# Kernel tuning notes

Measured on AMD Instinct MI355X. Metric: run time of the kernel, lower is better.

The kernel has to match this reference:

```python
import jax, jax.numpy as jnp
import numpy as np

B, S, D, H, HD = 8, 1374, 384, 6, 64
NUM_PATCHES = 1369  # (518 // 14) ** 2
NUM_PREFIX = 5      # 1 cls + 4 registers


def setup_inputs() -> dict:
    key = jax.random.key(0)
    ks = jax.random.split(key, 10)
    init = 0.02  # truncated_normal(0.02) approximated by scaled normal
    x = jax.random.normal(ks[0], (B, S, D), jnp.float32)
    wq = jax.random.truncated_normal(ks[1], -2.0, 2.0, (D, H, HD), jnp.float32) * init
    wk = jax.random.truncated_normal(ks[2], -2.0, 2.0, (D, H, HD), jnp.float32) * init
    wv = jax.random.truncated_normal(ks[3], -2.0, 2.0, (D, H, HD), jnp.float32) * init
    wo = jax.random.truncated_normal(ks[4], -2.0, 2.0, (H, HD, D), jnp.float32) * init
    bq = jnp.zeros((H, HD), jnp.float32)
    bk = jnp.zeros((H, HD), jnp.float32)
    bv = jnp.zeros((H, HD), jnp.float32)
    bo = jnp.zeros((D,), jnp.float32)
    keep_patch_indices = jax.random.randint(ks[5], (B, NUM_PATCHES), 0, NUM_PATCHES).astype(jnp.int64)
    return {"x": x, "wq": wq, "bq": bq, "wk": wk, "bk": bk, "wv": wv, "bv": bv,
            "wo": wo, "bo": bo, "keep_patch_indices": keep_patch_indices, "k_patches": 685}


def reference(x, wq, bq, wk, bk, wv, bv, wo, bo, keep_patch_indices, k_patches):
    # q/k/v projections: DenseGeneral to (heads, head_dim)
    q = jnp.einsum('bsd,dhe->bshe', x, wq) + bq
    k = jnp.einsum('bsd,dhe->bshe', x, wk) + bk
    v = jnp.einsum('bsd,dhe->bshe', x, wv) + bv

    z = jnp.einsum('bqhd,bkhd->bhqk', q / (HD ** 0.5), k)  # [B,H,S,S]
    attn_logits = z  # saved BEFORE masking (used by 'mse' criterion)

    # dynamic scatter mask: patch columns >= k_patches get -inf
    num_selected = keep_patch_indices.shape[1]
    patch_idx = jnp.arange(num_selected)
    indices_to_mask = jnp.where(patch_idx >= k_patches, patch_idx, num_selected) + NUM_PREFIX
    # out-of-bounds indices (== num_selected + NUM_PREFIX) are dropped by JAX scatter semantics
    z = z.at[:, :, :, indices_to_mask].set(-jnp.inf)

    attn_map = jax.nn.softmax(z, axis=-1)
    zo = jnp.einsum('bhqk,bkhd->bqhd', attn_map, v)
    output = jnp.einsum('bqhd,hdo->bqo', zo, wo) + bo  # wo contracts (heads, head_dim)

    # attn_aggregate = ['cls_token','reg_token','patch_token'], zoom_map_criterion='mse'
    am = attn_logits.mean(axis=1)  # mean over heads -> [B,S,S]
    aggs = jnp.stack([
        am[:, 0:1, :].mean(axis=1),      # cls token
        am[:, 1:5, :].mean(axis=1),      # register tokens
        am[:, 5:1374, :].mean(axis=1),   # patch tokens
    ], axis=1)                            # [B,3,S]
    attn_agg = aggs.mean(axis=1)          # [B,S]
    return output, attn_agg
```

## Files before the change

kernel.cpp:

```cpp
#include <hip/hip_runtime.h>
#include <stdint.h>

#define BB 8
#define SS 1374
#define DD 384
#define HH 6
#define HDIM 64
#define MROWS (BB*SS)
#define NPFX 5
#define SPAD 1376

typedef __attribute__((ext_vector_type(8))) short bf16x8;
typedef __attribute__((ext_vector_type(4))) float f32x4;
typedef __attribute__((ext_vector_type(4))) unsigned int u32x4;
typedef u32x4 __attribute__((aligned(4))) u32x4_u;

__device__ __forceinline__ unsigned short f2bf(float f){
  union { float f; unsigned int u; } v; v.f = f;
  return (unsigned short)((v.u + 0x7FFFu + ((v.u >> 16) & 1u)) >> 16);
}
__device__ __forceinline__ float bf2f(unsigned short b){
  union { float f; unsigned int u; } v; v.u = ((unsigned int)b) << 16; return v.f;
}
__device__ __forceinline__ unsigned int pk_bf16(float a, float b){
#if __has_builtin(__builtin_amdgcn_cvt_pk_bf16_f32)
  typedef __attribute__((ext_vector_type(2))) __bf16 bfv2;
  bfv2 p = __builtin_amdgcn_cvt_pk_bf16_f32(a, b);
  union { bfv2 v; unsigned int u; } c; c.v = p; return c.u;
#else
  return (unsigned int)f2bf(a) | ((unsigned int)f2bf(b) << 16);
#endif
}

__device__ __forceinline__ int xcd_remap(int i, int n){
  int q = n >> 3, r = n & 7;
  int x = i & 7, j = i >> 3;
  return (x < r ? x*(q+1) : r*(q+1) + (x - r)*q) + j;
}

__global__ void k_prep(const float* __restrict__ x, unsigned short* __restrict__ xb,
                       float* __restrict__ xbar){
  int b = blockIdx.x / 86, ch = blockIdx.x % 86;
  int d = threadIdx.x;
  int s0 = ch*16, s1 = s0 + 16; if (s1 > SS) s1 = SS;
  float acc = 0.f;
  for (int s = s0; s < s1; ++s){
    float v = x[((size_t)b*SS + s)*DD + d];
    float w = (s == 0) ? (1.f/3.f) : (s < 5) ? (1.f/12.f) : (1.f/4107.f);
    acc += w * v;
    xb[((size_t)b*SS + s)*DD + d] = f2bf(v);
  }
  atomicAdd(&xbar[b*DD + d], acc);
}

__global__ __launch_bounds__(256) void k_wtrans(const float* __restrict__ wq,
    const float* __restrict__ wk, const float* __restrict__ wv, const float* __restrict__ wo,
    unsigned short* __restrict__ wbT, unsigned short* __restrict__ woT){
  __shared__ float tile[32][33];
  int bid = blockIdx.x;
  int m = bid / 144, tl = bid % 144;
  int tr = tl / 12, tc = tl % 12;
  const float* src = (m==0) ? wq : (m==1) ? wk : (m==2) ? wv : wo;
  unsigned short* dst = (m < 3) ? (wbT + (size_t)m*384*384) : woT;
  int t = threadIdx.x, c = t & 31, r0 = t >> 5;
  #pragma unroll
  for (int p = 0; p < 4; ++p){
    int r = p*8 + r0;
    tile[r][c] = src[(size_t)(tr*32 + r)*384 + tc*32 + c];
  }
  __syncthreads();
  #pragma unroll
  for (int p = 0; p < 4; ++p){
    int r = p*8 + r0;
    dst[(size_t)(tc*32 + r)*384 + tr*32 + c] = f2bf(tile[c][r]);
  }
}

__global__ void k_qbar(const float* __restrict__ xbar, const float* __restrict__ wq,
                       const float* __restrict__ bq, float* __restrict__ qbar){
  __shared__ float xs[DD];
  int b = blockIdx.x / 6, nc = blockIdx.x % 6;
  int t = threadIdx.x;
  for (int i = t; i < DD; i += 64) xs[i] = xbar[b*DD + i];
  __syncthreads();
  int n = nc*64 + t;
  float acc = bq[n];
  for (int d = 0; d < DD; ++d) acc += xs[d]*wq[(size_t)d*384 + n];
  qbar[b*384 + n] = acc;
}

template<int MODE>
__global__ __launch_bounds__(256) void k_gemm(
    const unsigned short* __restrict__ A, const unsigned short* __restrict__ Bt,
    const float* __restrict__ b0, const float* __restrict__ b1, const float* __restrict__ b2,
    unsigned short* __restrict__ qg, unsigned short* __restrict__ kgp,
    unsigned short* __restrict__ vt, float* __restrict__ out,
    const int* __restrict__ kpat, const float* __restrict__ qbar, float* __restrict__ oagg)
{
  const int NT = (MODE==0) ? 18 : 6;
  int wg = xcd_remap(blockIdx.x, 86*NT);
  int mt = wg / NT, nt = wg % NT;
  const int t = threadIdx.x;
  const int w = t >> 6, lane = t & 63, quad = lane >> 4, l16 = lane & 15;
  const int wm = w >> 1, wn = w & 1;
  const int m0 = mt*128, n0 = nt*64;

  if (MODE == 0 && nt >= 12){
    int s0r_ = m0 % SS;
    int SKv = NPFX + kpat[0]; if (SKv > SS) SKv = SS; if (SKv < 1) SKv = 1;
    int lo = (SKv + 63) & ~63;
    if (s0r_ >= lo && s0r_ + 127 < SS) return;
  }

  constexpr int SMEM_SH = (MODE==0) ? 13824 : 17408;
  __shared__ unsigned short smem[SMEM_SH];
  unsigned short* As = smem;
  unsigned short* Bs = smem + 9216;
  f32x4 acc[4][2];
  #pragma unroll
  for (int i=0;i<4;i++){ acc[i][0] = (f32x4){0,0,0,0}; acc[i][1] = (f32x4){0,0,0,0}; }

  const int ar = t >> 1, akb = (t & 1) * 32;
  int ga = m0 + ar; if (ga > MROWS-1) ga = MROWS-1;
  const unsigned short* ap = A + (size_t)ga*384 + akb;
  const int br = t >> 2, bkb = (t & 3) * 16;
  const unsigned short* bp = Bt + (size_t)(n0 + br)*384 + bkb;

  u32x4 ra[4], rb[2];
  #pragma unroll
  for (int i=0;i<4;i++) ra[i] = *(const u32x4*)(ap + i*8);
  rb[0] = *(const u32x4*)(bp); rb[1] = *(const u32x4*)(bp + 8);

  for (int kc = 0; kc < 6; ++kc){
    asm volatile("s_waitcnt lgkmcnt(0)" ::: "memory");
    __builtin_amdgcn_s_barrier();
    #pragma unroll
    for (int i=0;i<4;i++) *(u32x4*)(As + ar*72 + akb + i*8) = ra[i];
    *(u32x4*)(Bs + br*72 + bkb)     = rb[0];
    *(u32x4*)(Bs + br*72 + bkb + 8) = rb[1];
    asm volatile("s_waitcnt lgkmcnt(0)" ::: "memory");
    __builtin_amdgcn_s_barrier();
    if (kc + 1 < 6){
      int kn = (kc+1)*64;
      #pragma unroll
      for (int i=0;i<4;i++) ra[i] = *(const u32x4*)(ap + kn + i*8);
      rb[0] = *(const u32x4*)(bp + kn); rb[1] = *(const u32x4*)(bp + kn + 8);
    }
    #pragma unroll
    for (int kh = 0; kh < 2; ++kh){
      bf16x8 af[4], bfr[2];
      #pragma unroll
      for (int rf = 0; rf < 4; ++rf)
        af[rf] = *(const bf16x8*)(As + (wm*64 + rf*16 + l16)*72 + kh*32 + quad*8);
      #pragma unroll
      for (int cf = 0; cf < 2; ++cf)
        bfr[cf] = *(const bf16x8*)(Bs + (wn*32 + cf*16 + l16)*72 + kh*32 + quad*8);
      #pragma unroll
      for (int rf = 0; rf < 4; ++rf)
        #pragma unroll
        for (int cf = 0; cf < 2; ++cf)
          acc[rf][cf] = __builtin_amdgcn_mfma_f32_16x16x32_bf16(af[rf], bfr[cf], acc[rf][cf], 0,0,0);
    }
  }

  const int b0r = m0 / SS, s0r = m0 % SS;
  __syncthreads();
  if (MODE == 1){
    float* CsF = (float*)smem;
    #pragma unroll
    for (int cf = 0; cf < 2; ++cf){
      int e = wn*32 + cf*16 + l16;
      float bias = b0[n0 + e];
      #pragma unroll
      for (int rf = 0; rf < 4; ++rf){
        int rr = wm*64 + rf*16 + quad*4;
        #pragma unroll
        for (int r4 = 0; r4 < 4; ++r4)
          CsF[(rr + r4)*68 + e] = acc[rf][cf][r4] + bias;
      }
    }
    __syncthreads();
    #pragma unroll
    for (int p = 0; p < 8; ++p){
      int r = p*16 + (t >> 4), c = t & 15;
      int rr = m0 + r;
      if (rr < MROWS){
        f32x4 v = *(const f32x4*)(CsF + r*68 + c*4);
        *(f32x4*)(out + (size_t)rr*384 + n0 + c*4) = v;
      }
    }
  } else {
    const int mat = nt / 6, h = nt - mat*6;
    const float* bvp = (mat==0) ? b0 : (mat==1) ? b1 : b2;
    const float vsc = (mat==0) ? 0.125f : 1.f;
    if (mat < 2){
      unsigned short* Cs = As;
      unsigned short* dst = (mat==0) ? qg : kgp;
      #pragma unroll
      for (int cf = 0; cf < 2; ++cf){
        int e = wn*32 + cf*16 + l16;
        float bias = bvp[h*64 + e];
        #pragma unroll
        for (int rf = 0; rf < 4; ++rf){
          int rr = wm*64 + rf*16 + quad*4;
          #pragma unroll
          for (int r4 = 0; r4 < 4; ++r4)
            Cs[(rr + r4)*72 + e] = f2bf((acc[rf][cf][r4] + bias)*vsc);
        }
      }
      __syncthreads();
      #pragma unroll
      for (int p = 0; p < 4; ++p){
        int r = p*32 + (t >> 3), c = t & 7;
        int rr = m0 + r;
        if (rr < MROWS){
          int s = s0r + r, bb = b0r;
          if (s >= SS){ s -= SS; ++bb; }
          u32x4 v = *(const u32x4*)(Cs + r*72 + c*8);
          *(u32x4*)(dst + (((size_t)(bb*HH + h))*SS + s)*64 + c*8) = v;
          if (mat == 1){
            const float* qh = qbar + bb*384 + h*64 + c*8;
            float part = 0.f;
            #pragma unroll
            for (int j = 0; j < 4; ++j){
              unsigned int u = v[j];
              part += qh[2*j]     * bf2f((unsigned short)(u & 0xFFFFu));
              part += qh[2*j + 1] * bf2f((unsigned short)(u >> 16));
            }
            part += __shfl_xor(part, 1);
            part += __shfl_xor(part, 2);
            part += __shfl_xor(part, 4);
            if (c == 0) atomicAdd(oagg + bb*SS + s, part * (1.f/48.f));
          }
        }
      }
    } else {
      unsigned short* CsV = As;
      #pragma unroll
      for (int cf = 0; cf < 2; ++cf){
        int e = wn*32 + cf*16 + l16;
        float bias = bvp[h*64 + e];
        #pragma unroll
        for (int rf = 0; rf < 4; ++rf){
          int rr = wm*64 + rf*16 + quad*4;
          #pragma unroll
          for (int p = 0; p < 2; ++p)
            *(unsigned int*)(CsV + e*136 + rr + p*2) =
                pk_bf16(acc[rf][cf][p*2] + bias, acc[rf][cf][p*2+1] + bias);
        }
      }
      __syncthreads();
      const bool nowrap = (s0r + 127 < SS) && (m0 + 127 < MROWS);
      if (nowrap){
        int e = t >> 2;
        unsigned short* vrow = vt + ((size_t)(b0r*HH + h)*64 + e)*SPAD + s0r;
        #pragma unroll
        for (int i = 0; i < 4; ++i){
          int c = (t & 3)*4 + i;
          u32x4 v = *(const u32x4*)(CsV + e*136 + c*8);
          *(u32x4_u*)(vrow + c*8) = v;
        }
      } else {
        for (int idx = t; idx < 64*64; idx += 256){
          int e = idx >> 6, sp = (idx & 63)*2;
          int rr = m0 + sp;
          if (rr < MROWS){
            int s = s0r + sp, bb = b0r;
            if (s >= SS){ s -= SS; ++bb; }
            *(unsigned int*)(vt + ((size_t)(bb*HH + h)*64 + e)*SPAD + s) =
                *(const unsigned int*)(CsV + e*136 + sp);
          }
        }
      }
    }
  }
}

#define KSTR 72
__global__ __launch_bounds__(256) void k_attn(
    const unsigned short* __restrict__ qg, const unsigned short* __restrict__ kg,
    const unsigned short* __restrict__ vt, unsigned short* __restrict__ zo,
    const int* __restrict__ kpat)
{
  const int NQB = 22;
  int wg = xcd_remap(blockIdx.x, 48*NQB);
  int qb = wg % NQB, bh = wg / NQB;
  int t = threadIdx.x, w = t >> 6, lane = t & 63, quad = lane >> 4, l16 = lane & 15;
  int SK = NPFX + kpat[0]; if (SK > SS) SK = SS; if (SK < 1) SK = 1;
  int niter = (SK + 63) >> 6;
  __shared__ unsigned short Ks[2][64*KSTR];
  __shared__ unsigned short Vs[2][64*KSTR];
  __shared__ unsigned short Ps[4][16*KSTR];
  unsigned short* Pw = &Ps[w][0];
  int q0 = qb*64 + w*16;

  bf16x8 aq[2];
  {
    int qrow = q0 + l16; if (qrow > SS-1) qrow = SS-1;
    const unsigned short* p = qg + ((size_t)bh*SS + qrow)*64;
    aq[0] = *(const bf16x8*)(p + quad*8);
    aq[1] = *(const bf16x8*)(p + 32 + quad*8);
  }
  f32x4 o[4];
  float rsum[4] = {0.f,0.f,0.f,0.f};
  #pragma unroll
  for (int i=0;i<4;i++) o[i] = (f32x4){0.f,0.f,0.f,0.f};

  const int srow = t >> 2, sc = (t & 3) * 16;
  const unsigned short* kbase = kg + ((size_t)bh*SS)*64;
  const unsigned short* vbase = vt + ((size_t)bh*64)*SPAD;
  u32x4 rk[2], rv[2];
  {
    rk[0] = *(const u32x4*)(kbase + (size_t)srow*64 + sc);
    rk[1] = *(const u32x4*)(kbase + (size_t)srow*64 + sc + 8);
    rv[0] = *(const u32x4*)(vbase + (size_t)srow*SPAD + sc);
    rv[1] = *(const u32x4*)(vbase + (size_t)srow*SPAD + sc + 8);
  }

  for (int it = 0; it < niter; ++it){
    int k0 = it*64;
    int cur = it & 1;
    unsigned short* Ksc = &Ks[cur][0];
    unsigned short* Vsc = &Vs[cur][0];
    *(u32x4*)(Ksc + srow*KSTR + sc)     = rk[0];
    *(u32x4*)(Ksc + srow*KSTR + sc + 8) = rk[1];
    *(u32x4*)(Vsc + srow*KSTR + sc)     = rv[0];
    *(u32x4*)(Vsc + srow*KSTR + sc + 8) = rv[1];
    if (it + 1 < niter){
      int kn = k0 + 64;
      int krow = kn + srow; if (krow > SS-1) krow = SS-1;
      rk[0] = *(const u32x4*)(kbase + (size_t)krow*64 + sc);
      rk[1] = *(const u32x4*)(kbase + (size_t)krow*64 + sc + 8);
      rv[0] = *(const u32x4*)(vbase + (size_t)srow*SPAD + kn + sc);
      rv[1] = *(const u32x4*)(vbase + (size_t)srow*SPAD + kn + sc + 8);
    }
    asm volatile("s_waitcnt lgkmcnt(0)" ::: "memory");
    __builtin_amdgcn_s_barrier();

    bool tail = (k0 + 64 > SK);
    #pragma unroll
    for (int ks = 0; ks < 2; ++ks){
      float pp[2][4];
      bf16x8 bkf[2][2];
      #pragma unroll
      for (int ns = 0; ns < 2; ++ns)
        #pragma unroll
        for (int ec = 0; ec < 2; ++ec)
          bkf[ns][ec] = *(const bf16x8*)(Ksc + (ks*32 + 2*l16 + ns)*KSTR + ec*32 + quad*8);
      __builtin_amdgcn_s_setprio(1);
      f32x4 z0 = (f32x4){0.f,0.f,0.f,0.f};
      f32x4 z1 = (f32x4){0.f,0.f,0.f,0.f};
      z0 = __builtin_amdgcn_mfma_f32_16x16x32_bf16(aq[0], bkf[0][0], z0, 0,0,0);
      z0 = __builtin_amdgcn_mfma_f32_16x16x32_bf16(aq[1], bkf[0][1], z0, 0,0,0);
      z1 = __builtin_amdgcn_mfma_f32_16x16x32_bf16(aq[0], bkf[1][0], z1, 0,0,0);
      z1 = __builtin_amdgcn_mfma_f32_16x16x32_bf16(aq[1], bkf[1][1], z1, 0,0,0);
      __builtin_amdgcn_s_setprio(0);
      bool v0 = !tail || (k0 + ks*32 + 2*l16)     < SK;
      bool v1 = !tail || (k0 + ks*32 + 2*l16 + 1) < SK;
      #pragma unroll
      for (int rg = 0; rg < 4; ++rg){
        pp[0][rg] = v0 ? __expf(z0[rg]) : 0.f;
        pp[1][rg] = v1 ? __expf(z1[rg]) : 0.f;
      }
      #pragma unroll
      for (int rg = 0; rg < 4; ++rg){
        rsum[rg] += pp[0][rg] + pp[1][rg];
        *(unsigned int*)(Pw + (quad*4 + rg)*KSTR + ks*32 + 2*l16) =
            pk_bf16(pp[0][rg], pp[1][rg]);
      }
    }
    #pragma unroll
    for (int kc = 0; kc < 2; ++kc){
      bf16x8 ap = *(const bf16x8*)(Pw + l16*KSTR + kc*32 + quad*8);
      __builtin_amdgcn_s_setprio(1);
      #pragma unroll
      for (int nc = 0; nc < 4; ++nc){
        bf16x8 vf = *(const bf16x8*)(Vsc + (nc*16 + l16)*KSTR + kc*32 + quad*8);
        o[nc] = __builtin_amdgcn_mfma_f32_16x16x32_bf16(ap, vf, o[nc], 0,0,0);
      }
      __builtin_amdgcn_s_setprio(0);
    }
  }
  int b = bh / HH, h = bh - (bh/HH)*HH;
  #pragma unroll
  for (int rg = 0; rg < 4; ++rg){
    float s = rsum[rg];
    #pragma unroll
    for (int off = 8; off >= 1; off >>= 1) s += __shfl_xor(s, off);
    int q = q0 + quad*4 + rg;
    if (q >= SS) continue;
    float inv = 1.f / s;
    unsigned short* dst = zo + ((size_t)b*SS + q)*384 + h*64;
    #pragma unroll
    for (int nc = 0; nc < 4; ++nc) dst[nc*16 + l16] = f2bf(o[nc][rg]*inv);
  }
}

extern "C" void kernel_launch(void* const* d_in, const int* in_sizes, int n_in,
                              void* d_out, int out_size, void* d_ws, size_t ws_size,
                              hipStream_t stream){
  const float* x  = (const float*)d_in[0];
  const float* wq = (const float*)d_in[1];
  const float* bq = (const float*)d_in[2];
  const float* wk = (const float*)d_in[3];
  const float* bk = (const float*)d_in[4];
  const float* wv = (const float*)d_in[5];
  const float* bv = (const float*)d_in[6];
  const float* wo = (const float*)d_in[7];
  const float* bo = (const float*)d_in[8];
  const int* kpat = (const int*)d_in[10];
  float* out = (float*)d_out;
  float* out_agg = out + (size_t)MROWS*DD;

  char* ws = (char*)d_ws;
  unsigned short* xb  = (unsigned short*)(ws);
  unsigned short* wbT = (unsigned short*)(ws +  8441856);
  unsigned short* woT = (unsigned short*)(ws +  9326592);
  unsigned short* qg  = (unsigned short*)(ws +  9621504);
  unsigned short* kg  = (unsigned short*)(ws + 18063360);
  unsigned short* vt  = (unsigned short*)(ws + 26505216);
  unsigned short* zo  = (unsigned short*)(ws + 34959360);
  float* xbar         = (float*)(ws + 43401216);
  float* qbar         = (float*)(ws + 43413504);
  (void)in_sizes; (void)n_in; (void)out_size; (void)ws_size;

  hipMemsetAsync(xbar, 0, BB*DD*sizeof(float), stream);
  hipMemsetAsync(out_agg, 0, BB*SS*sizeof(float), stream);
  k_prep<<<BB*86, 384, 0, stream>>>(x, xb, xbar);
  k_wtrans<<<576, 256, 0, stream>>>(wq, wk, wv, wo, wbT, woT);
  k_qbar<<<48, 64, 0, stream>>>(xbar, wq, bq, qbar);
  k_gemm<0><<<86*18, 256, 0, stream>>>(xb, wbT, bq, bk, bv, qg, kg, vt, nullptr, kpat, qbar, out_agg);
  k_attn<<<48*22, 256, 0, stream>>>(qg, kg, vt, zo, kpat);
  k_gemm<1><<<86*6, 256, 0, stream>>>(zo, woT, bo, nullptr, nullptr, nullptr, nullptr, nullptr, out, nullptr, nullptr, nullptr);
}
```

Measured before the change: 172.6 us.

## Merge prep, weight transpose and qbar into fewer launches; drop memsets and atomics

Folds the x bf16 conversion, the partial column sums of x, and the weight transposes into one k_prep launch. The qbar projection moves into the K-projection GEMM epilogue, where each block recomputes it in shared memory. Per-head aggregate partials are written to a buffer without atomics and summed in the output GEMM epilogue. This removes two memsets, two kernel launches and the atomic contention, at the cost of redundant 384-length dot products in every K-tile block and a serialized loop in the epilogue.

```diff
diff --git a/kernel.cpp b/kernel.cpp
--- a/kernel.cpp
+++ b/kernel.cpp
@@ -38,55 +38,50 @@
   return (x < r ? x*(q+1) : r*(q+1) + (x - r)*q) + j;
 }
 
-__global__ void k_prep(const float* __restrict__ x, unsigned short* __restrict__ xb,
-                       float* __restrict__ xbar){
-  int b = blockIdx.x / 86, ch = blockIdx.x % 86;
-  int d = threadIdx.x;
-  int s0 = ch*16, s1 = s0 + 16; if (s1 > SS) s1 = SS;
-  float acc = 0.f;
-  for (int s = s0; s < s1; ++s){
-    float v = x[((size_t)b*SS + s)*DD + d];
-    float w = (s == 0) ? (1.f/3.f) : (s < 5) ? (1.f/12.f) : (1.f/4107.f);
-    acc += w * v;
-    xb[((size_t)b*SS + s)*DD + d] = f2bf(v);
-  }
-  atomicAdd(&xbar[b*DD + d], acc);
-}
-
-__global__ __launch_bounds__(256) void k_wtrans(const float* __restrict__ wq,
-    const float* __restrict__ wk, const float* __restrict__ wv, const float* __restrict__ wo,
-    unsigned short* __restrict__ wbT, unsigned short* __restrict__ woT){
-  __shared__ float tile[32][33];
-  int bid = blockIdx.x;
-  int m = bid / 144, tl = bid % 144;
-  int tr = tl / 12, tc = tl % 12;
-  const float* src = (m==0) ? wq : (m==1) ? wk : (m==2) ? wv : wo;
-  unsigned short* dst = (m < 3) ? (wbT + (size_t)m*384*384) : woT;
-  int t = threadIdx.x, c = t & 31, r0 = t >> 5;
-  #pragma unroll
-  for (int p = 0; p < 4; ++p){
-    int r = p*8 + r0;
-    tile[r][c] = src[(size_t)(tr*32 + r)*384 + tc*32 + c];
-  }
-  __syncthreads();
-  #pragma unroll
-  for (int p = 0; p < 4; ++p){
-    int r = p*8 + r0;
-    dst[(size_t)(tc*32 + r)*384 + tr*32 + c] = f2bf(tile[c][r]);
-  }
-}
-
-__global__ void k_qbar(const float* __restrict__ xbar, const float* __restrict__ wq,
-                       const float* __restrict__ bq, float* __restrict__ qbar){
-  __shared__ float xs[DD];
-  int b = blockIdx.x / 6, nc = blockIdx.x % 6;
-  int t = threadIdx.x;
-  for (int i = t; i < DD; i += 64) xs[i] = xbar[b*DD + i];
-  __syncthreads();
-  int n = nc*64 + t;
-  float acc = bq[n];
-  for (int d = 0; d < DD; ++d) acc += xs[d]*wq[(size_t)d*384 + n];
-  qbar[b*384 + n] = acc;
+__global__ void k_prep(const float* __restrict__ x, const float* __restrict__ wq,
+                       const float* __restrict__ wk, const float* __restrict__ wv,
+                       const float* __restrict__ wo,
+                       unsigned short* __restrict__ xb, float* __restrict__ xpart,
+                       unsigned short* __restrict__ wbT, unsigned short* __restrict__ woT){
+  int bid = blockIdx.x, t = threadIdx.x;
+  if (bid < 688){
+    int b = bid / 86, ch = bid % 86;
+    int d = t;
+    int s0 = ch*16, s1 = s0 + 16; if (s1 > SS) s1 = SS;
+    for (int s = s0; s < s1; ++s)
+      xb[((size_t)b*SS + s)*DD + d] = f2bf(x[((size_t)b*SS + s)*DD + d]);
+  } else if (bid < 752){
+    int ib = bid - 688;
+    int b = ib >> 3, c = ib & 7;
+    int d = t;
+    int s0 = c*172, s1 = s0 + 172; if (s1 > SS) s1 = SS;
+    float acc = 0.f;
+    for (int s = s0; s < s1; ++s){
+      float w = (s == 0) ? (1.f/3.f) : (s < 5) ? (1.f/12.f) : (1.f/4107.f);
+      acc += w * x[((size_t)b*SS + s)*DD + d];
+    }
+    xpart[(c*8 + b)*384 + d] = acc;
+  } else {
+    if (t >= 256) return;
+    __shared__ float tile[32][33];
+    int bid2 = bid - 752;
+    int m = bid2 / 144, tl = bid2 % 144;
+    int tr = tl / 12, tc = tl % 12;
+    const float* src = (m==0) ? wq : (m==1) ? wk : (m==2) ? wv : wo;
+    unsigned short* dst = (m < 3) ? (wbT + (size_t)m*384*384) : woT;
+    int c = t & 31, r0 = t >> 5;
+    #pragma unroll
+    for (int p = 0; p < 4; ++p){
+      int r = p*8 + r0;
+      tile[r][c] = src[(size_t)(tr*32 + r)*384 + tc*32 + c];
+    }
+    __syncthreads();
+    #pragma unroll
+    for (int p = 0; p < 4; ++p){
+      int r = p*8 + r0;
+      dst[(size_t)(tc*32 + r)*384 + tr*32 + c] = f2bf(tile[c][r]);
+    }
+  }
 }
 
 template<int MODE>
@@ -95,7 +90,8 @@
     const float* __restrict__ b0, const float* __restrict__ b1, const float* __restrict__ b2,
     unsigned short* __restrict__ qg, unsigned short* __restrict__ kgp,
     unsigned short* __restrict__ vt, float* __restrict__ out,
-    const int* __restrict__ kpat, const float* __restrict__ qbar, float* __restrict__ oagg)
+    const int* __restrict__ kpat, const float* __restrict__ xpart,
+    const float* __restrict__ wqf, float* __restrict__ agg6, float* __restrict__ oagg)
 {
   const int NT = (MODE==0) ? 18 : 6;
   int wg = xcd_remap(blockIdx.x, 86*NT);
@@ -189,6 +185,15 @@
         *(f32x4*)(out + (size_t)rr*384 + n0 + c*4) = v;
       }
     }
+    if (nt == 0 && t < 128){
+      int rr = m0 + t;
+      if (rr < MROWS){
+        float s = 0.f;
+        #pragma unroll
+        for (int hh = 0; hh < 6; ++hh) s += agg6[hh*MROWS + rr];
+        oagg[rr] = s * (1.f/48.f);
+      }
+    }
   } else {
     const int mat = nt / 6, h = nt - mat*6;
     const float* bvp = (mat==0) ? b0 : (mat==1) ? b1 : b2;
@@ -196,6 +201,9 @@
     if (mat < 2){
       unsigned short* Cs = As;
       unsigned short* dst = (mat==0) ? qg : kgp;
+      float* xbl = (float*)Bs;
+      float* qbl = ((float*)Bs) + 768;
+      const int bb1 = (b0r + 1 < BB) ? b0r + 1 : BB - 1;
       #pragma unroll
       for (int cf = 0; cf < 2; ++cf){
         int e = wn*32 + cf*16 + l16;
@@ -208,18 +216,36 @@
             Cs[(rr + r4)*72 + e] = f2bf((acc[rf][cf][r4] + bias)*vsc);
         }
       }
+      if (mat == 1){
+        for (int i = t; i < 768; i += 256){
+          int bbx = i / 384, d = i - bbx*384;
+          int bsel = bbx ? bb1 : b0r;
+          float s = 0.f;
+          #pragma unroll
+          for (int c8 = 0; c8 < 8; ++c8) s += xpart[(c8*8 + bsel)*384 + d];
+          xbl[bbx*384 + d] = s;
+        }
+      }
       __syncthreads();
+      if (mat == 1 && t < 128){
+        int bbx = t >> 6, e = t & 63;
+        float a = b0[h*64 + e];
+        for (int d = 0; d < 384; ++d) a += xbl[bbx*384 + d] * wqf[(size_t)d*384 + h*64 + e];
+        qbl[bbx*64 + e] = a;
+      }
+      if (mat == 1) __syncthreads();
       #pragma unroll
       for (int p = 0; p < 4; ++p){
         int r = p*32 + (t >> 3), c = t & 7;
         int rr = m0 + r;
         if (rr < MROWS){
           int s = s0r + r, bb = b0r;
-          if (s >= SS){ s -= SS; ++bb; }
+          int bbx = 0;
+          if (s >= SS){ s -= SS; ++bb; bbx = 1; }
           u32x4 v = *(const u32x4*)(Cs + r*72 + c*8);
           *(u32x4*)(dst + (((size_t)(bb*HH + h))*SS + s)*64 + c*8) = v;
           if (mat == 1){
-            const float* qh = qbar + bb*384 + h*64 + c*8;
+            const float* qh = qbl + bbx*64 + c*8;
             float part = 0.f;
             #pragma unroll
             for (int j = 0; j < 4; ++j){
@@ -230,7 +256,7 @@
             part += __shfl_xor(part, 1);
             part += __shfl_xor(part, 2);
             part += __shfl_xor(part, 4);
-            if (c == 0) atomicAdd(oagg + bb*SS + s, part * (1.f/48.f));
+            if (c == 0) agg6[h*MROWS + rr] = part;
           }
         }
       }
@@ -420,16 +446,12 @@
   unsigned short* kg  = (unsigned short*)(ws + 18063360);
   unsigned short* vt  = (unsigned short*)(ws + 26505216);
   unsigned short* zo  = (unsigned short*)(ws + 34959360);
-  float* xbar         = (float*)(ws + 43401216);
-  float* qbar         = (float*)(ws + 43413504);
+  float* xpart        = (float*)(ws + 43401216);
+  float* agg6         = (float*)(ws + 43499520);
   (void)in_sizes; (void)n_in; (void)out_size; (void)ws_size;
 
-  hipMemsetAsync(xbar, 0, BB*DD*sizeof(float), stream);
-  hipMemsetAsync(out_agg, 0, BB*SS*sizeof(float), stream);
-  k_prep<<<BB*86, 384, 0, stream>>>(x, xb, xbar);
-  k_wtrans<<<576, 256, 0, stream>>>(wq, wk, wv, wo, wbT, woT);
-  k_qbar<<<48, 64, 0, stream>>>(xbar, wq, bq, qbar);
-  k_gemm<0><<<86*18, 256, 0, stream>>>(xb, wbT, bq, bk, bv, qg, kg, vt, nullptr, kpat, qbar, out_agg);
+  k_prep<<<1328, 384, 0, stream>>>(x, wq, wk, wv, wo, xb, xpart, wbT, woT);
+  k_gemm<0><<<86*18, 256, 0, stream>>>(xb, wbT, bq, bk, bv, qg, kg, vt, nullptr, kpat, xpart, wq, agg6, nullptr);
   k_attn<<<48*22, 256, 0, stream>>>(qg, kg, vt, zo, kpat);
-  k_gemm<1><<<86*6, 256, 0, stream>>>(zo, woT, bo, nullptr, nullptr, nullptr, nullptr, nullptr, out, nullptr, nullptr, nullptr);
-}
+  k_gemm<1><<<86*6, 256, 0, stream>>>(zo, woT, bo, nullptr, nullptr, nullptr, nullptr, nullptr, out, nullptr, nullptr, nullptr, agg6, out_agg);
+}
```

After: 197.1 us. 14.2% more time.
